# Kernel optimization log

Measured on AMD Instinct MI355X. Metric: run time of the kernel, lower is better.

Reference implementation:

```python
import jax, jax.numpy as jnp
import numpy as np

ALPHA = 0.2  # LeakyReLU negative slope


def setup_inputs() -> dict:
    key = jax.random.key(0)
    ks = jax.random.split(key, 6)
    B, N, F_in, F_out, H = 16, 1024, 256, 256, 8
    h = jax.random.normal(ks[0], (B, N, F_in), dtype=jnp.float32)
    # Per-head Linear W: weight [F_out, F_in] + bias [F_out], stacked over heads
    W = jax.random.normal(ks[1], (H, F_out, F_in), dtype=jnp.float32) * (1.414 / np.sqrt(F_in))
    bW = jax.random.normal(ks[2], (H, F_out), dtype=jnp.float32) * 0.01
    # Per-head Linear A: weight [1, 2*F_out] split into a1 (acts on Whi) and a2 (acts on Whj), bias bA [1]
    a1 = jax.random.normal(ks[3], (H, F_out), dtype=jnp.float32) * (1.414 / np.sqrt(2 * F_out))
    a2 = jax.random.normal(ks[4], (H, F_out), dtype=jnp.float32) * (1.414 / np.sqrt(2 * F_out))
    bA = jax.random.normal(ks[5], (H,), dtype=jnp.float32) * 0.01
    return {"h": h, "W": W, "bW": bW, "a1": a1, "a2": a2, "bA": bA}


def reference(h, W, bW, a1, a2, bA):
    # h: [B,N,F_in], W: [H,F_out,F_in]
    B, N, _ = h.shape
    H, F_out, _ = W.shape
    Wh = jnp.einsum('bnf,hof->bhno', h, W) + bW[None, :, None, :]  # [B,H,N,F_out]
    # Additive score e_ij = a1.Wh_i + a2.Wh_j + bA  (decomposed; avoids N x N x 2F concat)
    ei = jnp.einsum('bhno,ho->bhn', Wh, a1)  # contribution of row node i
    ej = jnp.einsum('bhno,ho->bhn', Wh, a2)  # contribution of col node j
    e = ei[:, :, :, None] + ej[:, :, None, :] + bA[None, :, None, None]  # [B,H,N,N]
    e = jnp.where(e > 0, e, ALPHA * e)  # LeakyReLU
    att = jax.nn.softmax(e, axis=-1)  # softmax over neighbors j (dropout = identity in eval)
    aWh = jnp.einsum('bhij,bhjo->bhio', att, Wh)  # [B,H,N,F_out]
    out = jax.nn.relu(aWh)  # last=False branch
    out = out.transpose(0, 2, 1, 3).reshape(B, N, H * F_out)  # concat heads on feature dim
    return jax.nn.sigmoid(out)
```

## Files before the change

### kernel.cpp

```cpp
#include <hip/hip_runtime.h>


#define L2E 1.442695041f

typedef _Float16 half8 __attribute__((ext_vector_type(8)));
typedef __fp16 fp16x2 __attribute__((ext_vector_type(2)));
typedef float floatx4 __attribute__((ext_vector_type(4)));

#if __has_builtin(__builtin_amdgcn_exp2f)
#define EXP2F(x) __builtin_amdgcn_exp2f(x)
#else
#define EXP2F(x) exp2f(x)
#endif

#if __has_builtin(__builtin_amdgcn_rcpf)
#define RCPF(x) __builtin_amdgcn_rcpf(x)
#else
#define RCPF(x) (1.0f / (x))
#endif

static __device__ inline unsigned int pack2(float a, float b) {
    fp16x2 h = __builtin_amdgcn_cvt_pkrtz(a, b);
    return __builtin_bit_cast(unsigned int, h);
}

typedef __attribute__((address_space(1))) const void GV;
typedef __attribute__((address_space(3))) void LV;
static __device__ inline void load_lds16(const void* g, void* l) {
    __builtin_amdgcn_global_load_lds((GV*)g, (LV*)l, 16, 0, 0);
}

static __device__ inline int swz(int row, int c) {
    return (row << 6) + ((((c) ^ (row >> 1)) & 3) << 4);
}
static __device__ inline int swz128(int row, int c) {
    return (row << 7) + ((((c) ^ row) & 7) << 4);
}

__global__ __launch_bounds__(256, 3) void wh_kernel(
    const float* __restrict__ hin, const float* __restrict__ W,
    const float* __restrict__ bW, _Float16* __restrict__ WhT,
    const float* __restrict__ a1, const float* __restrict__ a2,
    float* __restrict__ eiP, float* __restrict__ ejP)
{
    const int bnt  = blockIdx.x;
    const int ot   = blockIdx.y;
    const int head = blockIdx.z;
    const int t    = threadIdx.x;
    const int wave = t >> 6, lane = t & 63;
    const int l15 = lane & 15, quad = lane >> 4;
    const int wmh = wave & 1, wnh = wave >> 1;

    __shared__ char smem[16384];
    _Float16* As = (_Float16*)smem;
    _Float16* Bs = (_Float16*)(smem + 8192);
    float* bWs   = (float*)smem;
    float* a1s   = (float*)(smem + 512);
    float* a2s   = (float*)(smem + 1024);
    float* part1 = (float*)(smem + 1536);
    float* part2 = (float*)(smem + 2560);

    const int o0 = ot * 128;
    const int bn0 = bnt * 128;
    floatx4 acc[4][4];
#pragma unroll
    for (int a = 0; a < 4; a++)
#pragma unroll
        for (int b = 0; b < 4; b++) acc[a][b] = (floatx4)0.0f;

    const int ar = t >> 1, ah = t & 1;
    const float* Wrow = W + (size_t)(head * 256 + o0 + ar) * 256 + ah * 16;
    const float* hrow = hin + (size_t)(bn0 + ar) * 256 + ah * 16;

    float4 pa0, pa1, pa2, pa3, pb0, pb1, pb2, pb3;
    {
        const float4* p4 = (const float4*)Wrow;
        pa0 = p4[0]; pa1 = p4[1]; pa2 = p4[2]; pa3 = p4[3];
        const float4* q4 = (const float4*)hrow;
        pb0 = q4[0]; pb1 = q4[1]; pb2 = q4[2]; pb3 = q4[3];
    }

    for (int f0 = 0; f0 < 256; f0 += 32) {
        __syncthreads();
        *(uint4*)((char*)As + swz(ar, 2 * ah)) =
            make_uint4(pack2(pa0.x, pa0.y), pack2(pa0.z, pa0.w),
                       pack2(pa1.x, pa1.y), pack2(pa1.z, pa1.w));
        *(uint4*)((char*)As + swz(ar, 2 * ah + 1)) =
            make_uint4(pack2(pa2.x, pa2.y), pack2(pa2.z, pa2.w),
                       pack2(pa3.x, pa3.y), pack2(pa3.z, pa3.w));
        *(uint4*)((char*)Bs + swz(ar, 2 * ah)) =
            make_uint4(pack2(pb0.x, pb0.y), pack2(pb0.z, pb0.w),
                       pack2(pb1.x, pb1.y), pack2(pb1.z, pb1.w));
        *(uint4*)((char*)Bs + swz(ar, 2 * ah + 1)) =
            make_uint4(pack2(pb2.x, pb2.y), pack2(pb2.z, pb2.w),
                       pack2(pb3.x, pb3.y), pack2(pb3.z, pb3.w));
        if (f0 < 224) {
            const float4* p4 = (const float4*)(Wrow + f0 + 32);
            pa0 = p4[0]; pa1 = p4[1]; pa2 = p4[2]; pa3 = p4[3];
            const float4* q4 = (const float4*)(hrow + f0 + 32);
            pb0 = q4[0]; pb1 = q4[1]; pb2 = q4[2]; pb3 = q4[3];
        }
        __syncthreads();
        half8 af[4], bf[4];
#pragma unroll
        for (int a = 0; a < 4; a++)
            af[a] = *(const half8*)((char*)As + swz(wmh * 64 + a * 16 + l15, quad));
#pragma unroll
        for (int b = 0; b < 4; b++)
            bf[b] = *(const half8*)((char*)Bs + swz(wnh * 64 + b * 16 + l15, quad));
#pragma unroll
        for (int a = 0; a < 4; a++)
#pragma unroll
            for (int b = 0; b < 4; b++)
                acc[a][b] = __builtin_amdgcn_mfma_f32_16x16x32_f16(af[a], bf[b], acc[a][b], 0, 0, 0);
    }

    __syncthreads();
    if (t < 128) {
        bWs[t] = bW[head * 256 + o0 + t];
        a1s[t] = a1[head * 256 + o0 + t];
        a2s[t] = a2[head * 256 + o0 + t];
    }
    __syncthreads();

    const int bidx = bn0 >> 10;
    const int nbase = bn0 & 1023;
#pragma unroll
    for (int b = 0; b < 4; b++) {
        const int bnl = wnh * 64 + b * 16 + l15;
        const int n = nbase + bnl;
        float p1 = 0.f, p2 = 0.f;
#pragma unroll
        for (int a = 0; a < 4; a++) {
#pragma unroll
            for (int r = 0; r < 4; r++) {
                int ol = wmh * 64 + a * 16 + quad * 4 + r;
                float v = acc[a][b][r] + bWs[ol];
                WhT[(((size_t)(bidx * 8 + head) * 256 + o0 + ol) << 10) + n] = (_Float16)v;
                p1 = fmaf(v, a1s[ol], p1);
                p2 = fmaf(v, a2s[ol], p2);
            }
        }
        p1 += __shfl_xor(p1, 16, 64); p1 += __shfl_xor(p1, 32, 64);
        p2 += __shfl_xor(p2, 16, 64); p2 += __shfl_xor(p2, 32, 64);
        if (lane < 16) {
            part1[wmh * 128 + bnl] = p1;
            part2[wmh * 128 + bnl] = p2;
        }
    }
    __syncthreads();
    if (t < 128) {
        float s1 = part1[t] + part1[128 + t];
        float s2 = part2[t] + part2[128 + t];
        const size_t idx = (size_t)(bidx * 8 + head) * 1024 + nbase + t;
        eiP[(size_t)ot * 131072 + idx] = s1;
        ejP[(size_t)ot * 131072 + idx] = s2;
    }
}

__global__ __launch_bounds__(256, 2) void pv_kernel(
    const _Float16* __restrict__ WhT, const float* __restrict__ eiP,
    const float* __restrict__ ejP, const float* __restrict__ bA,
    float* __restrict__ out)
{
    const int n_ = blockIdx.x;
    const int x_ = n_ & 7, k_ = n_ >> 3;
    const int bh = 16 * x_ + (k_ >> 3);
    const int it = k_ & 7;
    const int b = bh >> 3, head = bh & 7;
    const int t = threadIdx.x;
    const int wave = t >> 6, lane = t & 63;
    const int l15 = lane & 15, quad = lane >> 4;
    const int wmh = wave & 1, wnh = wave >> 1;

    __shared__ char smem[53776];
    _Float16* Ap = (_Float16*)smem;
    _Float16* Bp = (_Float16*)(smem + 16384);
    float* ejs  = (float*)(smem + 49152);
    float* lns  = (float*)(smem + 53248);
    float* wred = (float*)(smem + 53760);

    const float* ej0 = ejP + bh * 1024;
    const float* ej1 = ejP + 131072 + bh * 1024;
    float mx = -1e30f;
#pragma unroll
    for (int k = 0; k < 4; k++) {
        int idx = t + k * 256;
        float v = (ej0[idx] + ej1[idx]) * L2E;
        ejs[idx] = v;
        mx = fmaxf(mx, v);
    }
#pragma unroll
    for (int m = 32; m; m >>= 1) mx = fmaxf(mx, __shfl_xor(mx, m, 64));
    if (lane == 0) wred[wave] = mx;
    __syncthreads();
    float ejmax = fmaxf(fmaxf(wred[0], wred[1]), fmaxf(wred[2], wred[3]));

    const int i0 = it * 128;
    const int prow = t >> 1, pjh = t & 1;
    const float cip = (eiP[bh * 1024 + i0 + prow] +
                       eiP[131072 + bh * 1024 + i0 + prow] + bA[head]) * L2E;
    const float tmv = cip + ejmax;
    const float nm = -fmaxf(tmv, 0.2f * tmv);
    const float Ac = cip + nm;
    const float Bc = fmaf(0.2f, cip, nm);

    const int rsub = lane >> 3, cp7 = lane & 7;
    const _Float16* bsrc = WhT + ((size_t)bh << 18)
                         + ((size_t)(wave * 64 + rsub) << 10)
                         + ((cp7 ^ rsub) << 3);
    char* bdst0 = (char*)Bp + wave * 8192;

    floatx4 acc[4][8];
#pragma unroll
    for (int a = 0; a < 4; a++)
#pragma unroll
        for (int c = 0; c < 8; c++) acc[a][c] = (floatx4)0.0f;
    float lsum = 0.0f;

    for (int j0 = 0; j0 < 1024; j0 += 64) {
        __syncthreads();
#pragma unroll
        for (int q = 0; q < 8; q++)
            load_lds16(bsrc + j0 + q * 8192, bdst0 + q * 1024);
        {
            const float4* ejp4 = (const float4*)(ejs + j0 + pjh * 32);
#pragma unroll
            for (int q = 0; q < 4; q++) {
                float4 e4a = ejp4[2 * q], e4b = ejp4[2 * q + 1];
                float p[8];
                const float ev[8] = {e4a.x, e4a.y, e4a.z, e4a.w,
                                     e4b.x, e4b.y, e4b.z, e4b.w};
#pragma unroll
                for (int u = 0; u < 8; u++) {
                    float t1 = Ac + ev[u];
                    float t2 = fmaf(0.2f, ev[u], Bc);
                    p[u] = EXP2F(fmaxf(t1, t2));
                    lsum += p[u];
                }
                *(uint4*)((char*)Ap + swz128(prow, pjh * 4 + q)) =
                    make_uint4(pack2(p[0], p[1]), pack2(p[2], p[3]),
                               pack2(p[4], p[5]), pack2(p[6], p[7]));
            }
        }
        __syncthreads();
#pragma unroll
        for (int kk = 0; kk < 2; kk++) {
            half8 af[4], bf[8];
#pragma unroll
            for (int a = 0; a < 4; a++)
                af[a] = *(const half8*)((char*)Ap + swz128(wmh * 64 + a * 16 + l15, kk * 4 + quad));
#pragma unroll
            for (int c = 0; c < 8; c++)
                bf[c] = *(const half8*)((char*)Bp + swz128(wnh * 128 + c * 16 + l15, kk * 4 + quad));
#pragma unroll
            for (int a = 0; a < 4; a++)
#pragma unroll
                for (int c = 0; c < 8; c++)
                    acc[a][c] = __builtin_amdgcn_mfma_f32_16x16x32_f16(af[a], bf[c], acc[a][c], 0, 0, 0);
        }
    }

    lsum += __shfl_xor(lsum, 1, 64);
    if (pjh == 0) lns[prow] = lsum;
    __syncthreads();

    float rs[4][4];
#pragma unroll
    for (int a = 0; a < 4; a++)
#pragma unroll
        for (int r = 0; r < 4; r++)
            rs[a][r] = -L2E * RCPF(lns[wmh * 64 + a * 16 + quad * 4 + r]);

#pragma unroll
    for (int a = 0; a < 4; a++) {
#pragma unroll
        for (int c = 0; c < 8; c++) {
            int o = wnh * 128 + c * 16 + l15;
#pragma unroll
            for (int r = 0; r < 4; r++) {
                int i = i0 + wmh * 64 + a * 16 + quad * 4 + r;
                float tx = fminf(acc[a][c][r] * rs[a][r], 0.0f);
                float y = RCPF(1.0f + EXP2F(tx));
                out[((size_t)(b * 1024 + i) << 11) + head * 256 + o] = y;
            }
        }
    }
}

extern "C" void kernel_launch(void* const* d_in, const int* in_sizes, int n_in,
                              void* d_out, int out_size, void* d_ws, size_t ws_size,
                              hipStream_t stream)
{
    const float* h  = (const float*)d_in[0];
    const float* W  = (const float*)d_in[1];
    const float* bW = (const float*)d_in[2];
    const float* a1 = (const float*)d_in[3];
    const float* a2 = (const float*)d_in[4];
    const float* bA = (const float*)d_in[5];
    float* out = (float*)d_out;

    char* ws = (char*)d_ws;
    _Float16* WhT = (_Float16*)ws;
    float* eiP = (float*)(ws + 67108864);
    float* ejP = (float*)(ws + 67108864 + 1048576);

    hipLaunchKernelGGL(wh_kernel, dim3(128, 2, 8), dim3(256), 0, stream,
                       h, W, bW, WhT, a1, a2, eiP, ejP);
    hipLaunchKernelGGL(pv_kernel, dim3(1024), dim3(256), 0, stream,
                       WhT, eiP, ejP, bA, out);
}
```

Measured before the change: 278.0 us.

## Double-buffer P and V tiles in pv_kernel with one barrier per step

```diff
diff --git a/kernel.cpp b/kernel.cpp
--- a/kernel.cpp
+++ b/kernel.cpp
@@ -32,9 +32,6 @@
 
 static __device__ inline int swz(int row, int c) {
     return (row << 6) + ((((c) ^ (row >> 1)) & 3) << 4);
-}
-static __device__ inline int swz128(int row, int c) {
-    return (row << 7) + ((((c) ^ row) & 7) << 4);
 }
 
 __global__ __launch_bounds__(256, 3) void wh_kernel(
@@ -174,8 +171,8 @@
     const int wmh = wave & 1, wnh = wave >> 1;
 
     __shared__ char smem[53776];
-    _Float16* Ap = (_Float16*)smem;
-    _Float16* Bp = (_Float16*)(smem + 16384);
+    char* ApB = smem;
+    char* BpB = smem + 16384;
     float* ejs  = (float*)(smem + 49152);
     float* lns  = (float*)(smem + 53248);
     float* wred = (float*)(smem + 53760);
@@ -205,11 +202,11 @@
     const float Ac = cip + nm;
     const float Bc = fmaf(0.2f, cip, nm);
 
-    const int rsub = lane >> 3, cp7 = lane & 7;
+    const int rsub = lane >> 2, cp = lane & 3, perm = (rsub >> 1) & 3;
     const _Float16* bsrc = WhT + ((size_t)bh << 18)
                          + ((size_t)(wave * 64 + rsub) << 10)
-                         + ((cp7 ^ rsub) << 3);
-    char* bdst0 = (char*)Bp + wave * 8192;
+                         + ((cp ^ perm) << 3);
+    char* bdst0 = BpB + wave * 4096;
 
     floatx4 acc[4][8];
 #pragma unroll
@@ -218,41 +215,54 @@
         for (int c = 0; c < 8; c++) acc[a][c] = (floatx4)0.0f;
     float lsum = 0.0f;
 
-    for (int j0 = 0; j0 < 1024; j0 += 64) {
+    auto pgen = [&](int j0, int buf) {
+        char* Apb = ApB + buf * 8192;
+        const float4* ejp4 = (const float4*)(ejs + j0 + pjh * 16);
+#pragma unroll
+        for (int q = 0; q < 2; q++) {
+            float4 e4a = ejp4[2 * q], e4b = ejp4[2 * q + 1];
+            float p[8];
+            const float ev[8] = {e4a.x, e4a.y, e4a.z, e4a.w,
+                                 e4b.x, e4b.y, e4b.z, e4b.w};
+#pragma unroll
+            for (int u = 0; u < 8; u++) {
+                float t1 = Ac + ev[u];
+                float t2 = fmaf(0.2f, ev[u], Bc);
+                p[u] = EXP2F(fmaxf(t1, t2));
+                lsum += p[u];
+            }
+            *(uint4*)(Apb + swz(prow, pjh * 2 + q)) =
+                make_uint4(pack2(p[0], p[1]), pack2(p[2], p[3]),
+                           pack2(p[4], p[5]), pack2(p[6], p[7]));
+        }
+    };
+
+#pragma unroll
+    for (int q = 0; q < 4; q++)
+        load_lds16(bsrc + q * 16384, bdst0 + q * 1024);
+    pgen(0, 0);
+
+    for (int tt = 0; tt < 32; ++tt) {
         __syncthreads();
-#pragma unroll
-        for (int q = 0; q < 8; q++)
-            load_lds16(bsrc + j0 + q * 8192, bdst0 + q * 1024);
+        const int cur = tt & 1, nb = cur ^ 1;
+        if (tt < 31) {
+            const int j0n = (tt + 1) * 32;
+#pragma unroll
+            for (int q = 0; q < 4; q++)
+                load_lds16(bsrc + j0n + q * 16384,
+                           bdst0 + nb * 16384 + q * 1024);
+            pgen(j0n, nb);
+        }
         {
-            const float4* ejp4 = (const float4*)(ejs + j0 + pjh * 32);
-#pragma unroll
-            for (int q = 0; q < 4; q++) {
-                float4 e4a = ejp4[2 * q], e4b = ejp4[2 * q + 1];
-                float p[8];
-                const float ev[8] = {e4a.x, e4a.y, e4a.z, e4a.w,
-                                     e4b.x, e4b.y, e4b.z, e4b.w};
-#pragma unroll
-                for (int u = 0; u < 8; u++) {
-                    float t1 = Ac + ev[u];
-                    float t2 = fmaf(0.2f, ev[u], Bc);
-                    p[u] = EXP2F(fmaxf(t1, t2));
-                    lsum += p[u];
-                }
-                *(uint4*)((char*)Ap + swz128(prow, pjh * 4 + q)) =
-                    make_uint4(pack2(p[0], p[1]), pack2(p[2], p[3]),
-                               pack2(p[4], p[5]), pack2(p[6], p[7]));
-            }
-        }
-        __syncthreads();
-#pragma unroll
-        for (int kk = 0; kk < 2; kk++) {
+            const char* Apb = ApB + cur * 8192;
+            const char* Bpb = BpB + cur * 16384;
             half8 af[4], bf[8];
 #pragma unroll
             for (int a = 0; a < 4; a++)
-                af[a] = *(const half8*)((char*)Ap + swz128(wmh * 64 + a * 16 + l15, kk * 4 + quad));
+                af[a] = *(const half8*)(Apb + swz(wmh * 64 + a * 16 + l15, quad));
 #pragma unroll
             for (int c = 0; c < 8; c++)
-                bf[c] = *(const half8*)((char*)Bp + swz128(wnh * 128 + c * 16 + l15, kk * 4 + quad));
+                bf[c] = *(const half8*)(Bpb + swz(wnh * 128 + c * 16 + l15, quad));
 #pragma unroll
             for (int a = 0; a < 4; a++)
 #pragma unroll
```

Measured after the change: 285.5 us. +2.7%, slower.

## Pre-convert inputs to fp16 and double-buffer direct-to-LDS loads in Wh GEMM

Applied to the files above, without the earlier changes.

```diff
diff --git a/kernel.cpp b/kernel.cpp
--- a/kernel.cpp
+++ b/kernel.cpp
@@ -37,8 +37,23 @@
     return (row << 7) + ((((c) ^ row) & 7) << 4);
 }
 
+__global__ __launch_bounds__(256) void cvt_kernel(
+    const float* __restrict__ W, const float* __restrict__ hin,
+    _Float16* __restrict__ W16, _Float16* __restrict__ h16)
+{
+    const size_t i = ((size_t)blockIdx.x * 256 + threadIdx.x) * 8;
+    const float* src;
+    _Float16* dst;
+    if (i < 524288) { src = W + i;              dst = W16 + i; }
+    else            { src = hin + (i - 524288); dst = h16 + (i - 524288); }
+    float4 v0 = *(const float4*)src;
+    float4 v1 = *(const float4*)(src + 4);
+    *(uint4*)dst = make_uint4(pack2(v0.x, v0.y), pack2(v0.z, v0.w),
+                              pack2(v1.x, v1.y), pack2(v1.z, v1.w));
+}
+
 __global__ __launch_bounds__(256, 3) void wh_kernel(
-    const float* __restrict__ hin, const float* __restrict__ W,
+    const _Float16* __restrict__ W16, const _Float16* __restrict__ h16,
     const float* __restrict__ bW, _Float16* __restrict__ WhT,
     const float* __restrict__ a1, const float* __restrict__ a2,
     float* __restrict__ eiP, float* __restrict__ ejP)
@@ -51,9 +66,7 @@
     const int l15 = lane & 15, quad = lane >> 4;
     const int wmh = wave & 1, wnh = wave >> 1;
 
-    __shared__ char smem[16384];
-    _Float16* As = (_Float16*)smem;
-    _Float16* Bs = (_Float16*)(smem + 8192);
+    __shared__ char smem[32768];
     float* bWs   = (float*)smem;
     float* a1s   = (float*)(smem + 512);
     float* a2s   = (float*)(smem + 1024);
@@ -68,54 +81,50 @@
 #pragma unroll
         for (int b = 0; b < 4; b++) acc[a][b] = (floatx4)0.0f;
 
-    const int ar = t >> 1, ah = t & 1;
-    const float* Wrow = W + (size_t)(head * 256 + o0 + ar) * 256 + ah * 16;
-    const float* hrow = hin + (size_t)(bn0 + ar) * 256 + ah * 16;
-
-    float4 pa0, pa1, pa2, pa3, pb0, pb1, pb2, pb3;
-    {
-        const float4* p4 = (const float4*)Wrow;
-        pa0 = p4[0]; pa1 = p4[1]; pa2 = p4[2]; pa3 = p4[3];
-        const float4* q4 = (const float4*)hrow;
-        pb0 = q4[0]; pb1 = q4[1]; pb2 = q4[2]; pb3 = q4[3];
-    }
-
-    for (int f0 = 0; f0 < 256; f0 += 32) {
-        __syncthreads();
-        *(uint4*)((char*)As + swz(ar, 2 * ah)) =
-            make_uint4(pack2(pa0.x, pa0.y), pack2(pa0.z, pa0.w),
-                       pack2(pa1.x, pa1.y), pack2(pa1.z, pa1.w));
-        *(uint4*)((char*)As + swz(ar, 2 * ah + 1)) =
-            make_uint4(pack2(pa2.x, pa2.y), pack2(pa2.z, pa2.w),
-                       pack2(pa3.x, pa3.y), pack2(pa3.z, pa3.w));
-        *(uint4*)((char*)Bs + swz(ar, 2 * ah)) =
-            make_uint4(pack2(pb0.x, pb0.y), pack2(pb0.z, pb0.w),
-                       pack2(pb1.x, pb1.y), pack2(pb1.z, pb1.w));
-        *(uint4*)((char*)Bs + swz(ar, 2 * ah + 1)) =
-            make_uint4(pack2(pb2.x, pb2.y), pack2(pb2.z, pb2.w),
-                       pack2(pb3.x, pb3.y), pack2(pb3.z, pb3.w));
-        if (f0 < 224) {
-            const float4* p4 = (const float4*)(Wrow + f0 + 32);
-            pa0 = p4[0]; pa1 = p4[1]; pa2 = p4[2]; pa3 = p4[3];
-            const float4* q4 = (const float4*)(hrow + f0 + 32);
-            pb0 = q4[0]; pb1 = q4[1]; pb2 = q4[2]; pb3 = q4[3];
-        }
-        __syncthreads();
+    const int rsub = lane >> 2, cp = lane & 3, perm = (rsub >> 1) & 3;
+    const _Float16* asrc = W16
+        + ((size_t)(head * 256 + o0 + wave * 32 + rsub)) * 256 + ((cp ^ perm) << 3);
+    const _Float16* bsrc = h16
+        + ((size_t)(bn0 + wave * 32 + rsub)) * 256 + ((cp ^ perm) << 3);
+    char* adst0 = smem + wave * 2048;
+    char* bdst0 = smem + 8192 + wave * 2048;
+
+#pragma unroll
+    for (int q = 0; q < 2; q++) {
+        load_lds16(asrc + q * 4096, adst0 + q * 1024);
+        load_lds16(bsrc + q * 4096, bdst0 + q * 1024);
+    }
+    __syncthreads();
+
+    for (int tt = 0; tt < 8; ++tt) {
+        const int cur = tt & 1, nb = cur ^ 1;
+        const char* Asb = smem + cur * 16384;
+        const char* Bsb = smem + cur * 16384 + 8192;
         half8 af[4], bf[4];
 #pragma unroll
         for (int a = 0; a < 4; a++)
-            af[a] = *(const half8*)((char*)As + swz(wmh * 64 + a * 16 + l15, quad));
+            af[a] = *(const half8*)(Asb + swz(wmh * 64 + a * 16 + l15, quad));
 #pragma unroll
         for (int b = 0; b < 4; b++)
-            bf[b] = *(const half8*)((char*)Bs + swz(wnh * 64 + b * 16 + l15, quad));
+            bf[b] = *(const half8*)(Bsb + swz(wnh * 64 + b * 16 + l15, quad));
+        if (tt < 7) {
+            const int f0n = (tt + 1) * 32;
+#pragma unroll
+            for (int q = 0; q < 2; q++) {
+                load_lds16(asrc + f0n + q * 4096,
+                           adst0 + nb * 16384 + q * 1024);
+                load_lds16(bsrc + f0n + q * 4096,
+                           bdst0 + nb * 16384 + q * 1024);
+            }
+        }
 #pragma unroll
         for (int a = 0; a < 4; a++)
 #pragma unroll
             for (int b = 0; b < 4; b++)
                 acc[a][b] = __builtin_amdgcn_mfma_f32_16x16x32_f16(af[a], bf[b], acc[a][b], 0, 0, 0);
-    }
-
-    __syncthreads();
+        __syncthreads();
+    }
+
     if (t < 128) {
         bWs[t] = bW[head * 256 + o0 + t];
         a1s[t] = a1[head * 256 + o0 + t];
@@ -305,8 +314,14 @@
     float* eiP = (float*)(ws + 67108864);
     float* ejP = (float*)(ws + 67108864 + 1048576);
 
+    char* outB = (char*)d_out;
+    _Float16* W16 = (_Float16*)(outB + 134217728 - 8388608 - 1048576);
+    _Float16* h16 = (_Float16*)(outB + 134217728 - 8388608);
+
+    hipLaunchKernelGGL(cvt_kernel, dim3(2304), dim3(256), 0, stream,
+                       W, h, W16, h16);
     hipLaunchKernelGGL(wh_kernel, dim3(128, 2, 8), dim3(256), 0, stream,
-                       h, W, bW, WhT, a1, a2, eiP, ejP);
+                       W16, h16, bW, WhT, a1, a2, eiP, ejP);
     hipLaunchKernelGGL(pv_kernel, dim3(1024), dim3(256), 0, stream,
                        WhT, eiP, ejP, bA, out);
 }
```

Result: slower. 283.7 us (+2.0%).
